# Kernel optimization log

Measured on AMD Instinct MI355X. Metric: run time of the kernel, lower is better.

The kernel has to match this reference:

```python
import jax, jax.numpy as jnp
import numpy as np

B, C, D, H = 16, 64, 512, 8
SEQ_LEN, LABEL_LEN, PRED_LEN = 1024, 512, 512
DEC_LEN = LABEL_LEN + PRED_LEN
DFF, KSIZE, FACTOR = 2048, 25, 3
E_LAYERS, D_LAYERS = 2, 1


def _pos_emb(L, d):
    pos = np.arange(L, dtype=np.float32)[:, None]
    div = np.exp(np.arange(0, d, 2, dtype=np.float32) * (-np.log(10000.0) / d))
    pe = np.zeros((L, d), np.float32)
    pe[:, 0::2] = np.sin(pos * div)
    pe[:, 1::2] = np.cos(pos * div)
    return jnp.asarray(pe)


def moving_mean(x, k=KSIZE):
    # AvgPool1d(k, stride=1) with replicate padding of (k-1)//2 at both ends
    pad = (k - 1) // 2
    xp = jnp.concatenate([jnp.repeat(x[:, :1], pad, 1), x, jnp.repeat(x[:, -1:], pad, 1)], axis=1)
    cs = jnp.cumsum(xp, axis=1)
    cs = jnp.concatenate([jnp.zeros_like(cs[:, :1]), cs], axis=1)
    return (cs[:, k:] - cs[:, :-k]) / k


def series_decomp(x):
    mm = moving_mean(x)
    return x - mm, mm


def circ_conv3(x, W):
    # Conv1d kernel=3, circular padding=1, no bias. x [B,L,Cin], W [3,Cin,Cout]
    L = x.shape[1]
    xp = jnp.concatenate([x[:, -1:], x, x[:, :1]], axis=1)
    return sum(jnp.einsum('blc,cd->bld', xp[:, k:k + L], W[k]) for k in range(3))


def my_layernorm(x, g, b):
    # LayerNorm then subtract per-sample mean over the time axis (special seasonal layernorm)
    mu = x.mean(-1, keepdims=True)
    var = x.var(-1, keepdims=True)
    xh = (x - mu) / jnp.sqrt(var + 1e-5) * g + b
    return xh - xh.mean(axis=1, keepdims=True)


def autocorrelation(q, k, v):
    # q,k,v: [B,L,H,E]. FFT cross-correlation, top-k lag selection, time-delay aggregation.
    L = q.shape[1]
    qf = jnp.fft.rfft(q.transpose(0, 2, 3, 1), axis=-1)
    kf = jnp.fft.rfft(k.transpose(0, 2, 3, 1), axis=-1)
    corr = jnp.fft.irfft(qf * jnp.conj(kf), n=L, axis=-1)  # [B,H,E,L]
    top_k = int(FACTOR * np.log(L))
    w, delay = jax.lax.top_k(corr.mean(axis=(1, 2)), top_k)  # [B,K]
    tc = jax.nn.softmax(w, axis=-1)
    vp = v.transpose(0, 2, 3, 1)  # [B,H,E,L]
    base = jnp.arange(L)
    agg = jnp.zeros_like(vp)
    for i in range(top_k):  # small fixed K (= int(factor*log L) = 20)
        idx = (base[None, :] + delay[:, i:i + 1]) % L  # circular shift == gather on doubled values
        pattern = jnp.take_along_axis(vp, idx[:, None, None, :], axis=-1)
        agg = agg + pattern * tc[:, i][:, None, None, None]
    return agg.transpose(0, 3, 1, 2)  # [B,L,H,E]


def ac_layer(q_in, kv_in, Wq, bq, Wk, bk, Wv, bv, Wo, bo):
    Bb, L, _ = q_in.shape
    S = kv_in.shape[1]
    E = D // H
    q = (q_in @ Wq + bq).reshape(Bb, L, H, E)
    k = (kv_in @ Wk + bk).reshape(Bb, S, H, E)
    v = (kv_in @ Wv + bv).reshape(Bb, S, H, E)
    out = autocorrelation(q, k, v)  # L == S by construction here
    return out.reshape(Bb, L, D) @ Wo + bo


def _forward(x_enc, x_dec, enc_emb_w, dec_emb_w, enc_Wq, enc_bq, enc_Wk, enc_bk, enc_Wv, enc_bv, enc_Wo, enc_bo, enc_ff1, enc_ff2, enc_ng, enc_nb, dsa_Wq, dsa_bq, dsa_Wk, dsa_bk, dsa_Wv, dsa_bv, dsa_Wo, dsa_bo, dca_Wq, dca_bq, dca_Wk, dca_bk, dca_Wv, dca_bv, dca_Wo, dca_bo, dec_ff1, dec_ff2, dec_trend_w, proj_w, proj_b):
    mean = jnp.repeat(x_enc.mean(axis=1, keepdims=True), PRED_LEN, axis=1)
    zeros = jnp.zeros((x_dec.shape[0], PRED_LEN, x_dec.shape[2]), x_enc.dtype)
    seasonal_init, trend_init = series_decomp(x_enc)
    trend = jnp.concatenate([trend_init[:, -LABEL_LEN:], mean], axis=1)
    seasonal_init = jnp.concatenate([seasonal_init[:, -LABEL_LEN:], zeros], axis=1)
    # encoder (DataEmbedding_wo_temp = token circular conv + sinusoidal pos, dropout=0)
    x = circ_conv3(x_enc, enc_emb_w) + _pos_emb(SEQ_LEN, D)[None]
    for l in range(E_LAYERS):
        x = x + ac_layer(x, x, enc_Wq[l], enc_bq[l], enc_Wk[l], enc_bk[l], enc_Wv[l], enc_bv[l], enc_Wo[l], enc_bo[l])
        x, _ = series_decomp(x)
        y = jax.nn.gelu(x @ enc_ff1[l], approximate=False) @ enc_ff2[l]
        x, _ = series_decomp(x + y)
    enc_out = my_layernorm(x, enc_ng, enc_nb)
    # decoder
    xd = circ_conv3(seasonal_init, dec_emb_w) + _pos_emb(DEC_LEN, D)[None]
    for l in range(D_LAYERS):
        xd = xd + ac_layer(xd, xd, dsa_Wq[l], dsa_bq[l], dsa_Wk[l], dsa_bk[l], dsa_Wv[l], dsa_bv[l], dsa_Wo[l], dsa_bo[l])
        xd, t1 = series_decomp(xd)
        xd = xd + ac_layer(xd, enc_out, dca_Wq[l], dca_bq[l], dca_Wk[l], dca_bk[l], dca_Wv[l], dca_bv[l], dca_Wo[l], dca_bo[l])
        xd, t2 = series_decomp(xd)
        y = jax.nn.gelu(xd @ dec_ff1[l], approximate=False) @ dec_ff2[l]
        xd, t3 = series_decomp(xd + y)
        trend = trend + circ_conv3(t1 + t2 + t3, dec_trend_w[l])  # trend projection conv
    seasonal = xd @ proj_w + proj_b
    out = trend + seasonal
    return out[:, -PRED_LEN:]


def setup_inputs():
    key = jax.random.key(0)
    ks = iter(jax.random.split(key, 64))
    def n(shape, s=0.02):
        return jax.random.normal(next(ks), shape, jnp.float32) * s
    inp = {}
    inp['x_enc'] = jax.random.normal(next(ks), (B, SEQ_LEN, C), jnp.float32)
    inp['x_dec'] = jax.random.normal(next(ks), (B, DEC_LEN, C), jnp.float32)
    inp['enc_emb_w'] = n((3, C, D))
    inp['dec_emb_w'] = n((3, C, D))
    for p in ['Wq', 'Wk', 'Wv', 'Wo']:
        bp = p.replace('W', 'b')
        inp['enc_' + p] = n((E_LAYERS, D, D)); inp['enc_' + bp] = jnp.zeros((E_LAYERS, D))
        inp['dsa_' + p] = n((D_LAYERS, D, D)); inp['dsa_' + bp] = jnp.zeros((D_LAYERS, D))
        inp['dca_' + p] = n((D_LAYERS, D, D)); inp['dca_' + bp] = jnp.zeros((D_LAYERS, D))
    inp['enc_ff1'] = n((E_LAYERS, D, DFF)); inp['enc_ff2'] = n((E_LAYERS, DFF, D))
    inp['enc_ng'] = jnp.ones((D,), jnp.float32); inp['enc_nb'] = jnp.zeros((D,), jnp.float32)
    inp['dec_ff1'] = n((D_LAYERS, D, DFF)); inp['dec_ff2'] = n((D_LAYERS, DFF, D))
    inp['dec_trend_w'] = n((D_LAYERS, 3, D, C))
    inp['proj_w'] = n((D, C)); inp['proj_b'] = jnp.zeros((C,), jnp.float32)
    return inp


def reference(x_enc, x_dec, enc_emb_w, dec_emb_w, enc_Wq, enc_bq, enc_Wk, enc_bk, enc_Wv, enc_bv, enc_Wo, enc_bo, enc_ff1, enc_ff2, enc_ng, enc_nb, dsa_Wq, dsa_bq, dsa_Wk, dsa_bk, dsa_Wv, dsa_bv, dsa_Wo, dsa_bo, dca_Wq, dca_bq, dca_Wk, dca_bk, dca_Wv, dca_bv, dca_Wo, dca_bo, dec_ff1, dec_ff2, dec_trend_w, proj_w, proj_b):
    return _forward(x_enc, x_dec, enc_emb_w, dec_emb_w, enc_Wq, enc_bq, enc_Wk, enc_bk, enc_Wv, enc_bv, enc_Wo, enc_bo, enc_ff1, enc_ff2, enc_ng, enc_nb, dsa_Wq, dsa_bq, dsa_Wk, dsa_bk, dsa_Wv, dsa_bv, dsa_Wo, dsa_bo, dca_Wq, dca_bq, dca_Wk, dca_bk, dca_Wv, dca_bv, dca_Wo, dca_bo, dec_ff1, dec_ff2, dec_trend_w, proj_w, proj_b)
```

## Files before the change

### kernel.cpp

```cpp
#include <hip/hip_runtime.h>
#include <math.h>

#define B_   16
#define L_   1024
#define C_   64
#define D_   512
#define DFF_ 2048
#define TOPK_ 20

typedef float f4 __attribute__((ext_vector_type(4)));
typedef float f32x4 __attribute__((ext_vector_type(4)));
typedef short bf16x8 __attribute__((ext_vector_type(8)));
typedef unsigned short u16x8 __attribute__((ext_vector_type(8)));

__device__ __forceinline__ unsigned short f2bf(float f) {
    union { float f; unsigned u; } a; a.f = f;
    unsigned r = a.u + 0x7fff + ((a.u >> 16) & 1);
    return (unsigned short)(r >> 16);
}
__device__ __forceinline__ float bf2f(unsigned short h) {
    union { unsigned u; float f; } a; a.u = ((unsigned)h) << 16;
    return a.f;
}

__device__ __forceinline__ float gelu_fast(float c) {
    float z  = c * 0.70710678118654752f;
    float az = fabsf(z);
    float t  = __builtin_amdgcn_rcpf(fmaf(0.3275911f, az, 1.0f));
    float p  = fmaf(fmaf(fmaf(fmaf(1.061405429f, t, -1.453152027f), t,
                              1.421413741f), t, -0.284496736f), t, 0.254829592f) * t;
    float e  = __expf(-z * z);
    float ea = fmaf(-p, e, 1.0f);
    float er = copysignf(ea, z);
    return 0.5f * c * (1.0f + er);
}

__device__ __forceinline__ void gld16(const void* g, void* l) {
    __builtin_amdgcn_global_load_lds(
        (const __attribute__((address_space(1))) unsigned int*)g,
        (__attribute__((address_space(3))) unsigned int*)l, 16, 0, 0);
}


__global__ __launch_bounds__(256)
void gemm_bf16(const unsigned short* __restrict__ A, const unsigned short* __restrict__ Bt,
               float* __restrict__ Cf, unsigned short* __restrict__ Cb,
               unsigned short* __restrict__ Cl,
               const float* __restrict__ bias, int M, int N, int K, int flags, int nx)
{
    __shared__ unsigned short As0[128 * 32], As1[128 * 32];
    __shared__ unsigned short Bs0[128 * 32], Bs1[128 * 32];
    const int tid = threadIdx.x;
    const int wave = tid >> 6, lane = tid & 63;

    int total = gridDim.x;
    int h = blockIdx.x;
    int lidx = h;
    if ((total & 7) == 0) {
        int q = total >> 3;
        lidx = (h & 7) * q + (h >> 3);
    }
    const int bm = (lidx / nx) * 128, bn = (lidx % nx) * 128;
    const int wm = (wave >> 1) << 6, wn = (wave & 1) << 6;

    const int r0 = (wave << 5) + (lane >> 2);
    const int kq = (((lane & 3) ^ ((lane >> 3) & 3)) << 3);
    const unsigned short* Ap0 = A + (size_t)(bm + r0) * K + kq;
    const unsigned short* Ap1 = Ap0 + (size_t)16 * K;
    const unsigned short* Bp0 = Bt + (size_t)(bn + r0) * K + kq;
    const unsigned short* Bp1 = Bp0 + (size_t)16 * K;
    const int wo0 = (wave << 5) * 32, wo1 = ((wave << 5) + 16) * 32;

    const int la = lane & 15, h4 = lane >> 4;
    const int sw = (la >> 1) & 3;
    f32x4 acc[4][4] = {};

    for (int k0 = 0; k0 < K; k0 += 64) {
        gld16(Ap0 + k0, &As0[wo0]);      gld16(Ap1 + k0, &As0[wo1]);
        gld16(Bp0 + k0, &Bs0[wo0]);      gld16(Bp1 + k0, &Bs0[wo1]);
        gld16(Ap0 + k0 + 32, &As1[wo0]); gld16(Ap1 + k0 + 32, &As1[wo1]);
        gld16(Bp0 + k0 + 32, &Bs1[wo0]); gld16(Bp1 + k0 + 32, &Bs1[wo1]);
        __syncthreads();
        bf16x8 a[4], b[4];
#pragma unroll
        for (int i = 0; i < 4; ++i) {
            a[i] = *(const bf16x8*)&As0[(wm + i * 16 + la) * 32 + ((h4 ^ sw) << 3)];
            b[i] = *(const bf16x8*)&Bs0[(wn + i * 16 + la) * 32 + ((h4 ^ sw) << 3)];
        }
#pragma unroll
        for (int mi = 0; mi < 4; ++mi)
#pragma unroll
            for (int ni = 0; ni < 4; ++ni)
                acc[mi][ni] = __builtin_amdgcn_mfma_f32_16x16x32_bf16(a[mi], b[ni], acc[mi][ni], 0, 0, 0);
#pragma unroll
        for (int i = 0; i < 4; ++i) {
            a[i] = *(const bf16x8*)&As1[(wm + i * 16 + la) * 32 + ((h4 ^ sw) << 3)];
            b[i] = *(const bf16x8*)&Bs1[(wn + i * 16 + la) * 32 + ((h4 ^ sw) << 3)];
        }
#pragma unroll
        for (int mi = 0; mi < 4; ++mi)
#pragma unroll
            for (int ni = 0; ni < 4; ++ni)
                acc[mi][ni] = __builtin_amdgcn_mfma_f32_16x16x32_bf16(a[mi], b[ni], acc[mi][ni], 0, 0, 0);
        __syncthreads();
    }

#pragma unroll
    for (int mi = 0; mi < 4; ++mi) {
#pragma unroll
        for (int r = 0; r < 4; ++r) {
            int m = bm + wm + mi * 16 + h4 * 4 + r;
#pragma unroll
            for (int ni = 0; ni < 4; ++ni) {
                int n = bn + wn + ni * 16 + la;
                float c = acc[mi][ni][r];
                if (bias) c += bias[n];
                if (flags & 2) c = gelu_fast(c);
                size_t o = (size_t)m * N + n;
                if (Cf) { if (flags & 1) Cf[o] += c; else Cf[o] = c; }
                if (Cb) {
                    unsigned short hb = f2bf(c);
                    Cb[o] = hb;
                    if (Cl) Cl[o] = f2bf(c - bf2f(hb));
                }
            }
        }
    }
}

__global__ __launch_bounds__(512)
void gemm256_gelu(const unsigned short* __restrict__ A, const unsigned short* __restrict__ Bt,
                  unsigned short* __restrict__ Cb, int M, int N, int K, int nx)
{
    __shared__ unsigned short As[2][16384];
    __shared__ unsigned short Bs[2][16384];
    const int tid = threadIdx.x;
    const int wave = tid >> 6, lane = tid & 63;

    int total = gridDim.x;
    int h = blockIdx.x;
    int lidx = h;
    if ((total & 7) == 0) {
        int q = total >> 3;
        lidx = (h & 7) * q + (h >> 3);
    }
    const int bm = (lidx / nx) * 256, bn = (lidx % nx) * 256;
    const int wm = (wave >> 2) << 7, wn = (wave & 3) << 6;

    const int r0 = (wave << 5) + (lane >> 2);
    const int kq = (((lane & 3) ^ ((lane >> 3) & 3)) << 3);
    const unsigned short* Ap0 = A + (size_t)(bm + r0) * K + kq;
    const unsigned short* Ap1 = Ap0 + (size_t)16 * K;
    const unsigned short* Bp0 = Bt + (size_t)(bn + r0) * K + kq;
    const unsigned short* Bp1 = Bp0 + (size_t)16 * K;
    const int wo0 = (wave << 5) * 32, wo1 = ((wave << 5) + 16) * 32;

    const int la = lane & 15, h4 = lane >> 4;
    const int sw = (la >> 1) & 3;
    f32x4 acc[8][4] = {};

    gld16(Ap0, &As[0][wo0]);             gld16(Ap1, &As[0][wo1]);
    gld16(Bp0, &Bs[0][wo0]);             gld16(Bp1, &Bs[0][wo1]);
    gld16(Ap0 + 32, &As[0][8192 + wo0]); gld16(Ap1 + 32, &As[0][8192 + wo1]);
    gld16(Bp0 + 32, &Bs[0][8192 + wo0]); gld16(Bp1 + 32, &Bs[0][8192 + wo1]);
    __syncthreads();

    const int nt = K >> 6;
    for (int t = 0; t < nt; ++t) {
        if (t + 1 < nt) {
            const int k0 = (t + 1) << 6;
            const int nb2 = (t + 1) & 1;
            gld16(Ap0 + k0, &As[nb2][wo0]);             gld16(Ap1 + k0, &As[nb2][wo1]);
            gld16(Bp0 + k0, &Bs[nb2][wo0]);             gld16(Bp1 + k0, &Bs[nb2][wo1]);
            gld16(Ap0 + k0 + 32, &As[nb2][8192 + wo0]); gld16(Ap1 + k0 + 32, &As[nb2][8192 + wo1]);
            gld16(Bp0 + k0 + 32, &Bs[nb2][8192 + wo0]); gld16(Bp1 + k0 + 32, &Bs[nb2][8192 + wo1]);
        }
        const int cb = t & 1;
#pragma unroll
        for (int hh = 0; hh < 2; ++hh) {
            const int hb = hh << 13;
            bf16x8 a[8], b[4];
#pragma unroll
            for (int i = 0; i < 8; ++i)
                a[i] = *(const bf16x8*)&As[cb][hb + (wm + i * 16 + la) * 32 + ((h4 ^ sw) << 3)];
#pragma unroll
            for (int i = 0; i < 4; ++i)
                b[i] = *(const bf16x8*)&Bs[cb][hb + (wn + i * 16 + la) * 32 + ((h4 ^ sw) << 3)];
#pragma unroll
            for (int mi = 0; mi < 8; ++mi)
#pragma unroll
                for (int ni = 0; ni < 4; ++ni)
                    acc[mi][ni] = __builtin_amdgcn_mfma_f32_16x16x32_bf16(a[mi], b[ni], acc[mi][ni], 0, 0, 0);
        }
        __syncthreads();
    }

#pragma unroll
    for (int mi = 0; mi < 8; ++mi)
#pragma unroll
        for (int r = 0; r < 4; ++r) {
            int m = bm + wm + mi * 16 + h4 * 4 + r;
#pragma unroll
            for (int ni = 0; ni < 4; ++ni) {
                int n = bn + wn + ni * 16 + la;
                Cb[(size_t)m * N + n] = f2bf(gelu_fast(acc[mi][ni][r]));
            }
        }
}

__global__ __launch_bounds__(256)
void gemm_split(const unsigned short* __restrict__ A, const unsigned short* __restrict__ Bt,
                unsigned short* __restrict__ o0h, unsigned short* __restrict__ o0l, const float* __restrict__ b0,
                unsigned short* __restrict__ o1h, unsigned short* __restrict__ o1l, const float* __restrict__ b1,
                unsigned short* __restrict__ o2h, unsigned short* __restrict__ o2l, const float* __restrict__ b2,
                float* __restrict__ Gz, int M, int N, int K, int nx)
{
    __shared__ unsigned short As0[128 * 32], As1[128 * 32];
    __shared__ unsigned short Bs0[128 * 32], Bs1[128 * 32];
    const int tid = threadIdx.x;
    const int wave = tid >> 6, lane = tid & 63;

    int total = gridDim.x;
    int h = blockIdx.x;
    if (Gz && h < 64) Gz[h * 256 + tid] = 0.f;
    int lidx = h;
    if ((total & 7) == 0) {
        int q = total >> 3;
        lidx = (h & 7) * q + (h >> 3);
    }
    const int bm = (lidx / nx) * 128, bn = (lidx % nx) * 128;
    const int wm = (wave >> 1) << 6, wn = (wave & 1) << 6;

    const int sel = bn >> 9;
    unsigned short* oh = sel == 0 ? o0h : (sel == 1 ? o1h : o2h);
    unsigned short* ol = sel == 0 ? o0l : (sel == 1 ? o1l : o2l);
    const float* bias  = sel == 0 ? b0  : (sel == 1 ? b1  : b2);
    const int nb = bn & 511;

    const int r0 = (wave << 5) + (lane >> 2);
    const int kq = (((lane & 3) ^ ((lane >> 3) & 3)) << 3);
    const unsigned short* Ap0 = A + (size_t)(bm + r0) * K + kq;
    const unsigned short* Ap1 = Ap0 + (size_t)16 * K;
    const unsigned short* Bp0 = Bt + (size_t)(bn + r0) * K + kq;
    const unsigned short* Bp1 = Bp0 + (size_t)16 * K;
    const int wo0 = (wave << 5) * 32, wo1 = ((wave << 5) + 16) * 32;

    const int la = lane & 15, h4 = lane >> 4;
    const int sw = (la >> 1) & 3;
    f32x4 acc[4][4] = {};

    for (int k0 = 0; k0 < K; k0 += 64) {
        gld16(Ap0 + k0, &As0[wo0]);      gld16(Ap1 + k0, &As0[wo1]);
        gld16(Bp0 + k0, &Bs0[wo0]);      gld16(Bp1 + k0, &Bs0[wo1]);
        gld16(Ap0 + k0 + 32, &As1[wo0]); gld16(Ap1 + k0 + 32, &As1[wo1]);
        gld16(Bp0 + k0 + 32, &Bs1[wo0]); gld16(Bp1 + k0 + 32, &Bs1[wo1]);
        __syncthreads();
        bf16x8 a[4], b[4];
#pragma unroll
        for (int i = 0; i < 4; ++i) {
            a[i] = *(const bf16x8*)&As0[(wm + i * 16 + la) * 32 + ((h4 ^ sw) << 3)];
            b[i] = *(const bf16x8*)&Bs0[(wn + i * 16 + la) * 32 + ((h4 ^ sw) << 3)];
        }
#pragma unroll
        for (int mi = 0; mi < 4; ++mi)
#pragma unroll
            for (int ni = 0; ni < 4; ++ni)
                acc[mi][ni] = __builtin_amdgcn_mfma_f32_16x16x32_bf16(a[mi], b[ni], acc[mi][ni], 0, 0, 0);
#pragma unroll
        for (int i = 0; i < 4; ++i) {
            a[i] = *(const bf16x8*)&As1[(wm + i * 16 + la) * 32 + ((h4 ^ sw) << 3)];
            b[i] = *(const bf16x8*)&Bs1[(wn + i * 16 + la) * 32 + ((h4 ^ sw) << 3)];
        }
#pragma unroll
        for (int mi = 0; mi < 4; ++mi)
#pragma unroll
            for (int ni = 0; ni < 4; ++ni)
                acc[mi][ni] = __builtin_amdgcn_mfma_f32_16x16x32_bf16(a[mi], b[ni], acc[mi][ni], 0, 0, 0);
        __syncthreads();
    }

#pragma unroll
    for (int mi = 0; mi < 4; ++mi) {
#pragma unroll
        for (int r = 0; r < 4; ++r) {
            int m = bm + wm + mi * 16 + h4 * 4 + r;
#pragma unroll
            for (int ni = 0; ni < 4; ++ni) {
                int n2 = nb + wn + ni * 16 + la;
                float c = acc[mi][ni][r] + bias[n2];
                size_t o = (size_t)m * 512 + n2;
                unsigned short hb = f2bf(c);
                oh[o] = hb;
                if (ol) ol[o] = f2bf(c - bf2f(hb));
            }
        }
    }
}

__global__ __launch_bounds__(256)
void tcast_kernel(const float* __restrict__ W, unsigned short* __restrict__ Wt, int R, int Cc)
{
    __shared__ float t[32][33];
    int bx = blockIdx.x * 32, by = blockIdx.y * 32;
    int tx = threadIdx.x & 31, ty = threadIdx.x >> 5;
#pragma unroll
    for (int i = 0; i < 32; i += 8)
        t[ty + i][tx] = W[(size_t)(by + ty + i) * Cc + bx + tx];
    __syncthreads();
#pragma unroll
    for (int i = 0; i < 32; i += 8)
        Wt[(size_t)(bx + ty + i) * R + by + tx] = f2bf(t[tx][ty + i]);
}

struct P16 { const float* p[16]; };
__global__ __launch_bounds__(256)
void tcast_all(P16 srcs, unsigned short* __restrict__ dst)
{
    __shared__ float t[32][33];
    const float* W = srcs.p[blockIdx.z];
    unsigned short* Wt = dst + (size_t)blockIdx.z * 262144;
    int bx = blockIdx.x * 32, by = blockIdx.y * 32;
    int tx = threadIdx.x & 31, ty = threadIdx.x >> 5;
#pragma unroll
    for (int i = 0; i < 32; i += 8)
        t[ty + i][tx] = W[(size_t)(by + ty + i) * 512 + bx + tx];
    __syncthreads();
#pragma unroll
    for (int i = 0; i < 32; i += 8)
        Wt[(size_t)(bx + ty + i) * 512 + by + tx] = f2bf(t[tx][ty + i]);
}

__global__ __launch_bounds__(256)
void pegen_kernel(float* __restrict__ PE)
{
    int idx = blockIdx.x * blockDim.x + threadIdx.x;
    int n = idx & 511, l = idx >> 9;
    int i2 = n & ~1;
    float div = expf(-(float)i2 * 0.017988946039015984f);
    float ang = (float)l * div;
    PE[idx] = (n & 1) ? cosf(ang) : sinf(ang);
}

__global__ __launch_bounds__(256)
void emb_kernel(const float* __restrict__ A, const float* __restrict__ W,
                const float* __restrict__ PEt,
                float* __restrict__ Xo, unsigned short* __restrict__ Xb)
{
    __shared__ float As[66][68];
    __shared__ float Ws[3][64][64];
    const int tid = threadIdx.x;
    const int bn = blockIdx.x * 64, bm = blockIdx.y * 64;
    const int base = bm & ~1023;
    for (int i = tid; i < 66 * 64; i += 256) {
        int r = i >> 6, c = i & 63;
        int l = (bm - base) + r - 1;
        if (l < 0) l += 1024; else if (l >= 1024) l -= 1024;
        As[r][c] = A[(size_t)(base + l) * 64 + c];
    }
    for (int i = tid; i < 3 * 64 * 64; i += 256) {
        int tap = i >> 12, rem = i & 4095, k = rem >> 6, c = rem & 63;
        Ws[tap][k][c] = W[((size_t)tap * 64 + k) * 512 + bn + c];
    }
    __syncthreads();
    const int tx = tid & 15, ty = tid >> 4;
    float acc[4][4] = {};
    for (int tap = 0; tap < 3; ++tap)
        for (int k = 0; k < 64; ++k) {
            f4 bv = *(const f4*)&Ws[tap][k][tx * 4];
#pragma unroll
            for (int i = 0; i < 4; ++i) {
                float a = As[ty * 4 + i + tap][k];
#pragma unroll
                for (int j = 0; j < 4; ++j)
                    acc[i][j] = fmaf(a, bv[j], acc[i][j]);
            }
        }
#pragma unroll
    for (int i = 0; i < 4; ++i) {
        int m = bm + ty * 4 + i;
        int l = m & 1023;
#pragma unroll
        for (int j = 0; j < 4; ++j) {
            int n = bn + tx * 4 + j;
            float c = acc[i][j] + PEt[((size_t)l << 9) + n];
            size_t o = (size_t)m * 512 + n;
            Xo[o] = c;
            Xb[o] = f2bf(c);
        }
    }
}

__global__ __launch_bounds__(256)
void tail_kernel(const float* __restrict__ TSUM, const float* __restrict__ T1,
                 const float* __restrict__ Wt, const float* __restrict__ pw,
                 float* __restrict__ PC, float* __restrict__ PP)
{
    __shared__ float Ts[18][17];
    __shared__ float T1s[16][17];
    __shared__ float Ws[3][16][64];
    __shared__ float Ps[16][64];
    const int tid = threadIdx.x;
    const int bo = blockIdx.x * 16;
    const int kc = blockIdx.y;
    const int b = bo >> 9;
    const int lbase = (bo & 511) + 512;
    const size_t rowbase = (size_t)b << 10;
    const int tc4 = (tid & 15) * 4;
    const int tr = tid >> 4;
    const int kbeg = kc * 64, kend = kbeg + 64;
    float cacc[4] = {}, pacc[4] = {};

    for (int k0 = kbeg; k0 < kend; k0 += 16) {
        for (int i = tid; i < 18 * 16; i += 256) {
            int r = i >> 4, c = i & 15;
            int l = lbase + r - 1; if (l >= 1024) l -= 1024;
            Ts[r][c] = TSUM[(rowbase + l) * 512 + k0 + c];
        }
        {
            int r = tid >> 4, c = tid & 15;
            T1s[r][c] = T1[(rowbase + lbase + r) * 512 + k0 + c];
        }
        for (int i = tid; i < 3 * 16 * 16; i += 256) {
            int tap = i / 256, rem = i & 255, k = rem >> 4, c4 = (rem & 15) * 4;
            *(f4*)&Ws[tap][k][c4] = *(const f4*)&Wt[((size_t)tap * 512 + k0 + k) * 64 + c4];
        }
        if (tid < 256) {
            int k = tid >> 4, c4 = (tid & 15) * 4;
            *(f4*)&Ps[k][c4] = *(const f4*)&pw[(size_t)(k0 + k) * 64 + c4];
        }
        __syncthreads();
        for (int tap = 0; tap < 3; ++tap)
#pragma unroll
            for (int k = 0; k < 16; ++k) {
                f4 bv = *(const f4*)&Ws[tap][k][tc4];
                float a = Ts[tr + tap][k];
#pragma unroll
                for (int j = 0; j < 4; ++j)
                    cacc[j] = fmaf(a, bv[j], cacc[j]);
            }
#pragma unroll
        for (int k = 0; k < 16; ++k) {
            f4 bv = *(const f4*)&Ps[k][tc4];
            float a = T1s[tr][k];
#pragma unroll
            for (int j = 0; j < 4; ++j)
                pacc[j] = fmaf(a, bv[j], pacc[j]);
        }
        __syncthreads();
    }
    size_t o = ((size_t)kc * 8192 + (bo + tr)) * 64 + tc4;
    *(f4*)&PC[o] = *(f4*)cacc;
    *(f4*)&PP[o] = *(f4*)pacc;
}

__global__ __launch_bounds__(256)
void tailred_kernel(const float* __restrict__ PC, const float* __restrict__ PP,
                    const float* __restrict__ MEANC, const float* __restrict__ pb,
                    float* __restrict__ OUT)
{
    int idx = blockIdx.x * blockDim.x + threadIdx.x;
    int n = idx & 63;
    int b = idx >> 15;
    const size_t S = (size_t)8192 * 64;
    float cs = PC[idx];
    float ps = PP[idx];
#pragma unroll
    for (int s = 1; s < 8; ++s) {
        cs += PC[s * S + idx];
        ps += PP[s * S + idx];
    }
    OUT[idx] = (MEANC[(b << 6) + n] + cs) + (ps + pb[n]);
}

__global__ __launch_bounds__(256)
void corr_mfma(const unsigned short* __restrict__ Qh, const unsigned short* __restrict__ Ql,
               const unsigned short* __restrict__ Kh, const unsigned short* __restrict__ Kl,
               float* __restrict__ G)
{
    __shared__ unsigned short Qhs[128 * 32], Qls[128 * 32], Khs[128 * 32], Kls[128 * 32];
    __shared__ float diagw[4][256];
    const int tid = threadIdx.x;
    const int wave = tid >> 6, lane = tid & 63;

    const int i_ = blockIdx.x;
    const int x_ = i_ & 7, j_ = i_ >> 3;
    const int b = x_ + ((j_ >> 6) << 3);
    const int tile = j_ & 63;
    const int bt = (tile >> 3) * 128, bs = (tile & 7) * 128;

    const int wm = (wave >> 1) << 6, wn = (wave & 1) << 6;
    const size_t boff = (size_t)b << 19;

    const int r0 = (wave << 5) + (lane >> 2);
    const int kq = (((lane & 3) ^ ((lane >> 3) & 3)) << 3);
    const size_t g0 = boff + (size_t)(bt + r0) * 512 + kq;
    const size_t g1 = g0 + (size_t)16 * 512;
    const size_t p0 = boff + (size_t)(bs + r0) * 512 + kq;
    const size_t p1 = p0 + (size_t)16 * 512;
    unsigned short* qh0 = &Qhs[(wave << 5) * 32]; unsigned short* qh1 = &Qhs[((wave << 5) + 16) * 32];
    unsigned short* ql0 = &Qls[(wave << 5) * 32]; unsigned short* ql1 = &Qls[((wave << 5) + 16) * 32];
    unsigned short* kh0 = &Khs[(wave << 5) * 32]; unsigned short* kh1 = &Khs[((wave << 5) + 16) * 32];
    unsigned short* kl0 = &Kls[(wave << 5) * 32]; unsigned short* kl1 = &Kls[((wave << 5) + 16) * 32];

    float* dz = &diagw[0][0];
    dz[tid] = 0.f; dz[tid + 256] = 0.f; dz[tid + 512] = 0.f; dz[tid + 768] = 0.f;

    const int la = lane & 15, h4 = lane >> 4;
    const int sw = (la >> 1) & 3;
    f32x4 acc[4][4] = {};

    for (int k0 = 0; k0 < 512; k0 += 32) {
        gld16(Qh + g0 + k0, qh0); gld16(Qh + g1 + k0, qh1);
        gld16(Ql + g0 + k0, ql0); gld16(Ql + g1 + k0, ql1);
        gld16(Kh + p0 + k0, kh0); gld16(Kh + p1 + k0, kh1);
        gld16(Kl + p0 + k0, kl0); gld16(Kl + p1 + k0, kl1);
        __syncthreads();
        bf16x8 ah[4], al[4], bh[4], bl[4];
#pragma unroll
        for (int i = 0; i < 4; ++i) {
            int ro = (wm + i * 16 + la) * 32 + ((h4 ^ sw) << 3);
            int co = (wn + i * 16 + la) * 32 + ((h4 ^ sw) << 3);
            ah[i] = *(const bf16x8*)&Qhs[ro];
            al[i] = *(const bf16x8*)&Qls[ro];
            bh[i] = *(const bf16x8*)&Khs[co];
            bl[i] = *(const bf16x8*)&Kls[co];
        }
#pragma unroll
        for (int mi = 0; mi < 4; ++mi)
#pragma unroll
            for (int ni = 0; ni < 4; ++ni) {
                acc[mi][ni] = __builtin_amdgcn_mfma_f32_16x16x32_bf16(ah[mi], bh[ni], acc[mi][ni], 0, 0, 0);
                acc[mi][ni] = __builtin_amdgcn_mfma_f32_16x16x32_bf16(ah[mi], bl[ni], acc[mi][ni], 0, 0, 0);
                acc[mi][ni] = __builtin_amdgcn_mfma_f32_16x16x32_bf16(al[mi], bh[ni], acc[mi][ni], 0, 0, 0);
            }
        __syncthreads();
    }

    float rbin[7][4] = {};
#pragma unroll
    for (int mi = 0; mi < 4; ++mi)
#pragma unroll
        for (int ni = 0; ni < 4; ++ni)
#pragma unroll
            for (int r = 0; r < 4; ++r)
                rbin[mi - ni + 3][r] += acc[mi][ni][r];

    const int base = (wm - wn) + 4 * h4 - la + 127;
#pragma unroll
    for (int d = 0; d < 7; ++d)
#pragma unroll
        for (int r = 0; r < 4; ++r)
            atomicAdd(&diagw[wave][base + 16 * (d - 3) + r], rbin[d][r]);
    __syncthreads();
    if (tid < 255) {
        float s = diagw[0][tid] + diagw[1][tid] + diagw[2][tid] + diagw[3][tid];
        int n = (bt - bs + tid - 127) & 1023;
        atomicAdd(&G[(b << 10) + n], s);
    }
}

__global__ __launch_bounds__(256)
void topk_kernel(const float* __restrict__ G, int* __restrict__ delay,
                 float* __restrict__ tc)
{
    __shared__ float vals[1024];
    __shared__ float pw[4];
    __shared__ int   pwi[4];
    __shared__ float wsel[TOPK_];
    __shared__ int   isel[TOPK_];
    const int b = blockIdx.x, tid = threadIdx.x;
    const int lane = tid & 63, wid = tid >> 6;
    for (int i = tid; i < 1024; i += 256) vals[i] = G[(b << 10) + i] * (1.0f / 512.0f);
    __syncthreads();
    for (int it = 0; it < TOPK_; ++it) {
        float bv = -INFINITY; int bi = 0;
#pragma unroll
        for (int u = 0; u < 4; ++u) {
            int i = tid * 4 + u;
            float v = vals[i];
            if (v > bv) { bv = v; bi = i; }
        }
#pragma unroll
        for (int o = 32; o > 0; o >>= 1) {
            float ov = __shfl_xor(bv, o, 64);
            int   oi = __shfl_xor(bi, o, 64);
            if (ov > bv || (ov == bv && oi < bi)) { bv = ov; bi = oi; }
        }
        if (lane == 0) { pw[wid] = bv; pwi[wid] = bi; }
        __syncthreads();
        if (tid == 0) {
            float m = pw[0]; int mi = pwi[0];
#pragma unroll
            for (int t = 1; t < 4; ++t)
                if (pw[t] > m || (pw[t] == m && pwi[t] < mi)) { m = pw[t]; mi = pwi[t]; }
            wsel[it] = m; isel[it] = mi;
            vals[mi] = -INFINITY;
        }
        __syncthreads();
    }
    if (tid == 0) {
        float m = wsel[0];
#pragma unroll
        for (int i = 1; i < TOPK_; ++i) m = fmaxf(m, wsel[i]);
        float e[TOPK_], s = 0.f;
#pragma unroll
        for (int i = 0; i < TOPK_; ++i) { e[i] = expf(wsel[i] - m); s += e[i]; }
        float inv = 1.0f / s;
#pragma unroll
        for (int i = 0; i < TOPK_; ++i) {
            tc[b * TOPK_ + i] = e[i] * inv;
            delay[b * TOPK_ + i] = isel[i];
        }
    }
}

__global__ __launch_bounds__(256)
void agg_kernel(const unsigned short* __restrict__ V, const int* __restrict__ delay,
                const float* __restrict__ tc, unsigned short* __restrict__ out)
{
    __shared__ int   dls[TOPK_];
    __shared__ float tcs[TOPK_];
    int h = blockIdx.x, g = gridDim.x, lh = h;
    if ((g & 7) == 0) {
        int q = g >> 3;
        lh = (h & 7) * q + (h >> 3);
    }
    int idx = (lh * blockDim.x + threadIdx.x) * 8;
    int d = idx & 511;
    int l = (idx >> 9) & 1023;
    int b = idx >> 19;
    if (threadIdx.x < TOPK_) {
        dls[threadIdx.x] = delay[b * TOPK_ + threadIdx.x];
        tcs[threadIdx.x] = tc[b * TOPK_ + threadIdx.x];
    }
    __syncthreads();
    const unsigned short* Vb = V + ((size_t)b << 19);
    float s[8] = {};
#pragma unroll
    for (int i = 0; i < TOPK_; ++i) {
        int row = (l + dls[i]) & 1023;
        float w = tcs[i];
        u16x8 v = *(const u16x8*)&Vb[((size_t)row << 9) + d];
#pragma unroll
        for (int j = 0; j < 8; ++j)
            s[j] = fmaf(w, bf2f(v[j]), s[j]);
    }
    u16x8 o;
#pragma unroll
    for (int j = 0; j < 8; ++j) o[j] = f2bf(s[j]);
    *(u16x8*)&out[idx] = o;
}

__global__ void decomp_kernel(const float* __restrict__ x, float* __restrict__ seas,
                              unsigned short* __restrict__ seasb,
                              float* __restrict__ trend, int Bn, int Ln, int Ch,
                              int nseg, int tmode)
{
    int h = blockIdx.x, g = gridDim.x, lh = h;
    if ((g & 7) == 0) {
        int q = g >> 3;
        lh = (h & 7) * q + (h >> 3);
    }
    int idx = lh * blockDim.x + threadIdx.x;
    int total = Bn * Ch * nseg;
    if (idx >= total) return;
    int ch = idx % Ch;
    int rest = idx / Ch;
    int seg = rest % nseg;
    int b = rest / nseg;
    int segL = Ln / nseg;
    int l0 = seg * segL;
    const float* xp = x + (size_t)b * Ln * Ch + ch;
    float* sp = seas + (size_t)b * Ln * Ch + ch;
    unsigned short* bp = seasb ? seasb + (size_t)b * Ln * Ch + ch : nullptr;
    float* tp = trend ? trend + (size_t)b * Ln * Ch + ch : nullptr;
    float s = 0.f;
    for (int j = -12; j <= 12; ++j) {
        int t = l0 + j;
        t = t < 0 ? 0 : (t > Ln - 1 ? Ln - 1 : t);
        s += xp[(size_t)t * Ch];
    }
    for (int l = l0; l < l0 + segL; ++l) {
        float mm = s * (1.0f / 25.0f);
        float v = xp[(size_t)l * Ch] - mm;
        sp[(size_t)l * Ch] = v;
        if (bp) bp[(size_t)l * Ch] = f2bf(v);
        if (tmode == 1) tp[(size_t)l * Ch] = mm;
        else if (tmode == 2) tp[(size_t)l * Ch] += mm;
        int ta = l + 13; if (ta > Ln - 1) ta = Ln - 1;
        int ts = l - 12; if (ts < 0) ts = 0;
        s += xp[(size_t)ta * Ch] - xp[(size_t)ts * Ch];
    }
}

__global__ __launch_bounds__(256)
void lnrow_kernel(const float* __restrict__ x, const float* __restrict__ g,
                  const float* __restrict__ bv, float* __restrict__ out)
{
    __shared__ float sh1[4], sh2[4];
    int row = blockIdx.x, tid = threadIdx.x;
    const float* xr = x + ((size_t)row << 9);
    float v0 = xr[tid], v1 = xr[tid + 256];
    float s = v0 + v1, q = v0 * v0 + v1 * v1;
#pragma unroll
    for (int o = 32; o > 0; o >>= 1) {
        s += __shfl_down(s, o, 64);
        q += __shfl_down(q, o, 64);
    }
    int wid = tid >> 6;
    if ((tid & 63) == 0) { sh1[wid] = s; sh2[wid] = q; }
    __syncthreads();
    if (tid == 0) {
        sh1[0] = sh1[0] + sh1[1] + sh1[2] + sh1[3];
        sh2[0] = sh2[0] + sh2[1] + sh2[2] + sh2[3];
    }
    __syncthreads();
    float mu = sh1[0] * (1.0f / 512.0f);
    float var = sh2[0] * (1.0f / 512.0f) - mu * mu;
    float inv = rsqrtf(var + 1e-5f);
    out[((size_t)row << 9) + tid] = (v0 - mu) * inv * g[tid] + bv[tid];
    out[((size_t)row << 9) + tid + 256] = (v1 - mu) * inv * g[tid + 256] + bv[tid + 256];
}

__global__ void colmean_kernel(const float* __restrict__ x, float* __restrict__ m)
{
    int idx = blockIdx.x * blockDim.x + threadIdx.x;
    if (idx >= B_ * D_) return;
    int b = idx >> 9, d = idx & 511;
    const float* xp = x + ((size_t)b << 19) + d;
    float s = 0.f;
    for (int l = 0; l < L_; ++l) s += xp[(size_t)l << 9];
    m[idx] = s * (1.0f / 1024.0f);
}

__global__ void colsub_kernel(const float* __restrict__ x, const float* __restrict__ m,
                              unsigned short* __restrict__ out)
{
    int idx = blockIdx.x * blockDim.x + threadIdx.x;
    int d = idx & 511;
    int b = idx >> 19;
    out[idx] = f2bf(x[idx] - m[(b << 9) + d]);
}

__global__ void meanx_kernel(const float* __restrict__ x, float* __restrict__ m)
{
    int idx = blockIdx.x * blockDim.x + threadIdx.x;
    if (idx >= B_ * C_) return;
    int b = idx >> 6, c = idx & 63;
    const float* xp = x + (size_t)b * L_ * C_ + c;
    float s = 0.f;
    for (int l = 0; l < L_; ++l) s += xp[(size_t)l << 6];
    m[idx] = s * (1.0f / 1024.0f);
}

__global__ void builddec_kernel(const float* __restrict__ seenc, float* __restrict__ seasin)
{
    int idx = blockIdx.x * blockDim.x + threadIdx.x;
    int c = idx & 63;
    int l = (idx >> 6) & 1023;
    int b = idx >> 16;
    if (l < 512) {
        int src = (b << 16) + ((512 + l) << 6) + c;
        seasin[idx] = seenc[src];
    } else {
        seasin[idx] = 0.f;
    }
}

extern "C" void kernel_launch(void* const* d_in, const int* in_sizes, int n_in,
                              void* d_out, int out_size, void* d_ws, size_t ws_size,
                              hipStream_t stream)
{
    auto F = [&](int i) { return (const float*)d_in[i]; };
    const float* x_enc     = F(0);
    const float* enc_emb_w = F(2);
    const float* dec_emb_w = F(3);
    const float* enc_Wq = F(4);  const float* enc_bq = F(5);
    const float* dsa_Wq = F(6);  const float* dsa_bq = F(7);
    const float* dca_Wq = F(8);  const float* dca_bq = F(9);
    const float* enc_Wk = F(10); const float* enc_bk = F(11);
    const float* dsa_Wk = F(12); const float* dsa_bk = F(13);
    const float* dca_Wk = F(14); const float* dca_bk = F(15);
    const float* enc_Wv = F(16); const float* enc_bv = F(17);
    const float* dsa_Wv = F(18); const float* dsa_bv = F(19);
    const float* dca_Wv = F(20); const float* dca_bv = F(21);
    const float* enc_Wo = F(22); const float* enc_bo = F(23);
    const float* dsa_Wo = F(24); const float* dsa_bo = F(25);
    const float* dca_Wo = F(26); const float* dca_bo = F(27);
    const float* enc_ff1 = F(28); const float* enc_ff2 = F(29);
    const float* enc_ng = F(30);  const float* enc_nb = F(31);
    const float* dec_ff1 = F(32); const float* dec_ff2 = F(33);
    const float* dec_trend_w = F(34);
    const float* proj_w = F(35);  const float* proj_b = F(36);

    constexpr size_t F512 = (size_t)B_ * L_ * D_;
    constexpr size_t F64  = (size_t)B_ * L_ * C_;
    constexpr size_t SMALL = 1024 + 16384 + 320 + 320 + 8192;
    constexpr size_t WTSA_N = 16 * 262144;
    constexpr size_t WTSF_N = 2 * 1024 * 1024;
    size_t need = (3 * F512 + 2 * F64 + SMALL) * 4 + (8 * F512 + WTSA_N + WTSF_N) * 2;
    if (ws_size < need) return;

    float* X      = (float*)d_ws;
    float* T1     = X + F512;
    float* TSUM   = T1 + F512;
    float* SEASIN = TSUM + F512;
    float* PET    = SEASIN + F64;
    float* MEANC  = PET + F64;
    float* G      = MEANC + 1024;
    float* TCW    = G + 16384;
    int*   DEL    = (int*)(TCW + 320);
    float* LNMEAN = (float*)(DEL + 320);
    unsigned short* AB   = (unsigned short*)(LNMEAN + 8192);
    unsigned short* EB   = AB + F512;
    unsigned short* VB   = EB + F512;
    unsigned short* HB   = VB + F512;
    unsigned short* QHI  = HB + F512;
    unsigned short* QLO  = QHI + F512;
    unsigned short* KHI  = QLO + F512;
    unsigned short* KLO  = KHI + F512;
    unsigned short* WTSA = KLO + F512;
    unsigned short* WTSF = WTSA + WTSA_N;
    float* OUT = (float*)d_out;

    const int M = B_ * L_;

    auto mgemm = [&](const unsigned short* A, const unsigned short* Bt, float* Cf,
                     unsigned short* Cb, unsigned short* Cl, const float* bias,
                     int Mm, int Nn, int Kk, int flags) {
        int nx = Nn / 128;
        int total = nx * (Mm / 128);
        gemm_bf16<<<total, 256, 0, stream>>>(A, Bt, Cf, Cb, Cl, bias, Mm, Nn, Kk, flags, nx);
    };
    auto tcast = [&](const float* W, unsigned short* Wt, int R, int Cc) {
        tcast_kernel<<<dim3(Cc / 32, R / 32), 256, 0, stream>>>(W, Wt, R, Cc);
    };
    auto corr_topk_agg = [&]() {
        corr_mfma<<<1024, 256, 0, stream>>>(QHI, QLO, KHI, KLO, G);
        topk_kernel<<<16, 256, 0, stream>>>(G, DEL, TCW);
        agg_kernel<<<(int)(F512 / 8 / 256), 256, 0, stream>>>(VB, DEL, TCW, HB);
    };
    auto attn_self = [&](const unsigned short* xin, int slotbase,
                         const float* bq, const float* bk, const float* bvp, const float* bo,
                         float* resid) {
        gemm_split<<<12 * 128, 256, 0, stream>>>(xin, WTSA + (size_t)slotbase * 262144,
            QHI, QLO, bq, KHI, KLO, bk, VB, nullptr, bvp, G, M, 1536, 512, 12);
        corr_topk_agg();
        mgemm(HB, WTSA + (size_t)(slotbase + 3) * 262144, resid, nullptr, nullptr, bo, M, 512, 512, 1);
    };
    auto attn_cross = [&](const unsigned short* qin, const unsigned short* kvin, int slotbase,
                          const float* bq, const float* bk, const float* bvp, const float* bo,
                          float* resid) {
        mgemm(qin, WTSA + (size_t)slotbase * 262144, nullptr, QHI, QLO, bq, M, 512, 512, 0);
        gemm_split<<<8 * 128, 256, 0, stream>>>(kvin, WTSA + (size_t)(slotbase + 1) * 262144,
            KHI, KLO, bk, VB, nullptr, bvp, nullptr, nullptr, nullptr, G, M, 1024, 512, 8);
        corr_topk_agg();
        mgemm(HB, WTSA + (size_t)(slotbase + 3) * 262144, resid, nullptr, nullptr, bo, M, 512, 512, 1);
    };
    auto ffblock = [&](const unsigned short* xin, const float* W1, const float* W2, float* resid) {
        unsigned short* Wf1 = WTSF;
        unsigned short* Wf2 = WTSF + 1048576;
        unsigned short* HFULL = QHI;
        tcast(W1, Wf1, 512, 2048);
        tcast(W2, Wf2, 2048, 512);
        gemm256_gelu<<<512, 512, 0, stream>>>(xin, Wf1, HFULL, M, 2048, 512, 8);
        mgemm(HFULL, Wf2, resid, nullptr, nullptr, nullptr, M, 512, 2048, 1);
    };

    {
        P16 srcs;
        for (int l = 0; l < 2; ++l) {
            srcs.p[l * 4 + 0] = enc_Wq + (size_t)l * 262144;
            srcs.p[l * 4 + 1] = enc_Wk + (size_t)l * 262144;
            srcs.p[l * 4 + 2] = enc_Wv + (size_t)l * 262144;
            srcs.p[l * 4 + 3] = enc_Wo + (size_t)l * 262144;
        }
        srcs.p[8]  = dsa_Wq; srcs.p[9]  = dsa_Wk; srcs.p[10] = dsa_Wv; srcs.p[11] = dsa_Wo;
        srcs.p[12] = dca_Wq; srcs.p[13] = dca_Wk; srcs.p[14] = dca_Wv; srcs.p[15] = dca_Wo;
        tcast_all<<<dim3(16, 16, 16), 256, 0, stream>>>(srcs, WTSA);
    }
    pegen_kernel<<<2048, 256, 0, stream>>>(PET);

    float* SEENC = (float*)QHI;
    decomp_kernel<<<(B_ * C_ * 64 + 255) / 256, 256, 0, stream>>>(x_enc, SEENC, nullptr, nullptr, B_, L_, C_, 64, 0);
    meanx_kernel<<<(B_ * C_ + 255) / 256, 256, 0, stream>>>(x_enc, MEANC);
    builddec_kernel<<<(int)(F64 / 256), 256, 0, stream>>>(SEENC, SEASIN);

    emb_kernel<<<dim3(8, 256), 256, 0, stream>>>(x_enc, enc_emb_w, PET, X, AB);

    for (int l = 0; l < 2; ++l) {
        attn_self(AB, l * 4,
                  enc_bq + l * D_, enc_bk + l * D_, enc_bv + l * D_, enc_bo + l * D_, X);
        decomp_kernel<<<(B_ * D_ * 64 + 255) / 256, 256, 0, stream>>>(X, T1, AB, nullptr, B_, L_, D_, 64, 0);
        ffblock(AB, enc_ff1 + (size_t)l * D_ * DFF_, enc_ff2 + (size_t)l * DFF_ * D_, T1);
        decomp_kernel<<<(B_ * D_ * 64 + 255) / 256, 256, 0, stream>>>(T1, X, AB, nullptr, B_, L_, D_, 64, 0);
    }
    lnrow_kernel<<<M, 256, 0, stream>>>(X, enc_ng, enc_nb, T1);
    colmean_kernel<<<(B_ * D_ + 255) / 256, 256, 0, stream>>>(T1, LNMEAN);
    colsub_kernel<<<(int)(F512 / 256), 256, 0, stream>>>(T1, LNMEAN, EB);

    float* XD = X;
    emb_kernel<<<dim3(8, 256), 256, 0, stream>>>(SEASIN, dec_emb_w, PET, XD, AB);

    attn_self(AB, 8, dsa_bq, dsa_bk, dsa_bv, dsa_bo, XD);
    decomp_kernel<<<(B_ * D_ * 64 + 255) / 256, 256, 0, stream>>>(XD, T1, AB, TSUM, B_, L_, D_, 64, 1);

    attn_cross(AB, EB, 12, dca_bq, dca_bk, dca_bv, dca_bo, T1);
    decomp_kernel<<<(B_ * D_ * 64 + 255) / 256, 256, 0, stream>>>(T1, XD, AB, TSUM, B_, L_, D_, 64, 2);

    ffblock(AB, dec_ff1, dec_ff2, XD);
    decomp_kernel<<<(B_ * D_ * 64 + 255) / 256, 256, 0, stream>>>(XD, T1, nullptr, TSUM, B_, L_, D_, 64, 2);

    float* PART_C = (float*)QHI;
    float* PART_P = PART_C + (size_t)8 * 8192 * 64;
    tail_kernel<<<dim3(512, 8), 256, 0, stream>>>(TSUM, T1, dec_trend_w, proj_w, PART_C, PART_P);
    tailred_kernel<<<2048, 256, 0, stream>>>(PART_C, PART_P, MEANC, proj_b, OUT);
}
```

Baseline: 1.727 ms.

## Enlarge corr_mfma tile to 256x256 with double-buffered LDS prefetch

The correlation MFMA kernel now uses 512-thread blocks computing 256x256 tiles, with eight waves each owning 128x64, instead of 128x128 tiles. Each block fetches the next K slice into a second LDS buffer while computing on the current one, so only one barrier per iteration remains. The aim is to raise data reuse per global load, hide load latency, and reduce diagonal atomic traffic to G. In exchange, per-thread accumulator registers double and LDS use rises, while only 256 blocks are launched, which may lower occupancy and how many CUs are kept busy.

```diff
diff --git a/kernel.cpp b/kernel.cpp
--- a/kernel.cpp
+++ b/kernel.cpp
@@ -472,23 +472,23 @@
     OUT[idx] = (MEANC[(b << 6) + n] + cs) + (ps + pb[n]);
 }
 
-__global__ __launch_bounds__(256)
+__global__ __launch_bounds__(512)
 void corr_mfma(const unsigned short* __restrict__ Qh, const unsigned short* __restrict__ Ql,
                const unsigned short* __restrict__ Kh, const unsigned short* __restrict__ Kl,
                float* __restrict__ G)
 {
-    __shared__ unsigned short Qhs[128 * 32], Qls[128 * 32], Khs[128 * 32], Kls[128 * 32];
-    __shared__ float diagw[4][256];
+    __shared__ unsigned short Qhs[2][8192], Qls[2][8192], Khs[2][8192], Kls[2][8192];
+    __shared__ float diagw[8][512];
     const int tid = threadIdx.x;
     const int wave = tid >> 6, lane = tid & 63;
 
     const int i_ = blockIdx.x;
     const int x_ = i_ & 7, j_ = i_ >> 3;
-    const int b = x_ + ((j_ >> 6) << 3);
-    const int tile = j_ & 63;
-    const int bt = (tile >> 3) * 128, bs = (tile & 7) * 128;
-
-    const int wm = (wave >> 1) << 6, wn = (wave & 1) << 6;
+    const int b = x_ + ((j_ >> 4) << 3);
+    const int tile = j_ & 15;
+    const int bt = (tile >> 2) * 256, bs = (tile & 3) * 256;
+
+    const int wm = (wave >> 2) << 7, wn = (wave & 3) << 6;
     const size_t boff = (size_t)b << 19;
 
     const int r0 = (wave << 5) + (lane >> 2);
@@ -497,64 +497,92 @@
     const size_t g1 = g0 + (size_t)16 * 512;
     const size_t p0 = boff + (size_t)(bs + r0) * 512 + kq;
     const size_t p1 = p0 + (size_t)16 * 512;
-    unsigned short* qh0 = &Qhs[(wave << 5) * 32]; unsigned short* qh1 = &Qhs[((wave << 5) + 16) * 32];
-    unsigned short* ql0 = &Qls[(wave << 5) * 32]; unsigned short* ql1 = &Qls[((wave << 5) + 16) * 32];
-    unsigned short* kh0 = &Khs[(wave << 5) * 32]; unsigned short* kh1 = &Khs[((wave << 5) + 16) * 32];
-    unsigned short* kl0 = &Kls[(wave << 5) * 32]; unsigned short* kl1 = &Kls[((wave << 5) + 16) * 32];
-
-    float* dz = &diagw[0][0];
-    dz[tid] = 0.f; dz[tid + 256] = 0.f; dz[tid + 512] = 0.f; dz[tid + 768] = 0.f;
+    const int wo0 = (wave << 5) * 32, wo1 = ((wave << 5) + 16) * 32;
+
+    {
+        float* dz = &diagw[0][0];
+#pragma unroll
+        for (int i = 0; i < 8; ++i) dz[tid + i * 512] = 0.f;
+    }
 
     const int la = lane & 15, h4 = lane >> 4;
     const int sw = (la >> 1) & 3;
-    f32x4 acc[4][4] = {};
-
-    for (int k0 = 0; k0 < 512; k0 += 32) {
-        gld16(Qh + g0 + k0, qh0); gld16(Qh + g1 + k0, qh1);
-        gld16(Ql + g0 + k0, ql0); gld16(Ql + g1 + k0, ql1);
-        gld16(Kh + p0 + k0, kh0); gld16(Kh + p1 + k0, kh1);
-        gld16(Kl + p0 + k0, kl0); gld16(Kl + p1 + k0, kl1);
+    f32x4 acc[8][4] = {};
+
+    gld16(Qh + g0, &Qhs[0][wo0]); gld16(Qh + g1, &Qhs[0][wo1]);
+    gld16(Ql + g0, &Qls[0][wo0]); gld16(Ql + g1, &Qls[0][wo1]);
+    gld16(Kh + p0, &Khs[0][wo0]); gld16(Kh + p1, &Khs[0][wo1]);
+    gld16(Kl + p0, &Kls[0][wo0]); gld16(Kl + p1, &Kls[0][wo1]);
+    __syncthreads();
+
+    for (int t = 0; t < 16; ++t) {
+        if (t + 1 < 16) {
+            const int k0 = (t + 1) << 5;
+            const int nb2 = (t + 1) & 1;
+            gld16(Qh + g0 + k0, &Qhs[nb2][wo0]); gld16(Qh + g1 + k0, &Qhs[nb2][wo1]);
+            gld16(Ql + g0 + k0, &Qls[nb2][wo0]); gld16(Ql + g1 + k0, &Qls[nb2][wo1]);
+            gld16(Kh + p0 + k0, &Khs[nb2][wo0]); gld16(Kh + p1 + k0, &Khs[nb2][wo1]);
+            gld16(Kl + p0 + k0, &Kls[nb2][wo0]); gld16(Kl + p1 + k0, &Kls[nb2][wo1]);
+        }
+        const int cb = t & 1;
+        bf16x8 ah[8], bh[4];
+#pragma unroll
+        for (int i = 0; i < 8; ++i)
+            ah[i] = *(const bf16x8*)&Qhs[cb][(wm + i * 16 + la) * 32 + ((h4 ^ sw) << 3)];
+#pragma unroll
+        for (int i = 0; i < 4; ++i)
+            bh[i] = *(const bf16x8*)&Khs[cb][(wn + i * 16 + la) * 32 + ((h4 ^ sw) << 3)];
+#pragma unroll
+        for (int mi = 0; mi < 8; ++mi)
+#pragma unroll
+            for (int ni = 0; ni < 4; ++ni)
+                acc[mi][ni] = __builtin_amdgcn_mfma_f32_16x16x32_bf16(ah[mi], bh[ni], acc[mi][ni], 0, 0, 0);
+        {
+            bf16x8 bl[4];
+#pragma unroll
+            for (int i = 0; i < 4; ++i)
+                bl[i] = *(const bf16x8*)&Kls[cb][(wn + i * 16 + la) * 32 + ((h4 ^ sw) << 3)];
+#pragma unroll
+            for (int mi = 0; mi < 8; ++mi)
+#pragma unroll
+                for (int ni = 0; ni < 4; ++ni)
+                    acc[mi][ni] = __builtin_amdgcn_mfma_f32_16x16x32_bf16(ah[mi], bl[ni], acc[mi][ni], 0, 0, 0);
+        }
+        {
+            bf16x8 al[8];
+#pragma unroll
+            for (int i = 0; i < 8; ++i)
+                al[i] = *(const bf16x8*)&Qls[cb][(wm + i * 16 + la) * 32 + ((h4 ^ sw) << 3)];
+#pragma unroll
+            for (int mi = 0; mi < 8; ++mi)
+#pragma unroll
+                for (int ni = 0; ni < 4; ++ni)
+                    acc[mi][ni] = __builtin_amdgcn_mfma_f32_16x16x32_bf16(al[mi], bh[ni], acc[mi][ni], 0, 0, 0);
+        }
         __syncthreads();
-        bf16x8 ah[4], al[4], bh[4], bl[4];
-#pragma unroll
-        for (int i = 0; i < 4; ++i) {
-            int ro = (wm + i * 16 + la) * 32 + ((h4 ^ sw) << 3);
-            int co = (wn + i * 16 + la) * 32 + ((h4 ^ sw) << 3);
-            ah[i] = *(const bf16x8*)&Qhs[ro];
-            al[i] = *(const bf16x8*)&Qls[ro];
-            bh[i] = *(const bf16x8*)&Khs[co];
-            bl[i] = *(const bf16x8*)&Kls[co];
-        }
-#pragma unroll
-        for (int mi = 0; mi < 4; ++mi)
-#pragma unroll
-            for (int ni = 0; ni < 4; ++ni) {
-                acc[mi][ni] = __builtin_amdgcn_mfma_f32_16x16x32_bf16(ah[mi], bh[ni], acc[mi][ni], 0, 0, 0);
-                acc[mi][ni] = __builtin_amdgcn_mfma_f32_16x16x32_bf16(ah[mi], bl[ni], acc[mi][ni], 0, 0, 0);
-                acc[mi][ni] = __builtin_amdgcn_mfma_f32_16x16x32_bf16(al[mi], bh[ni], acc[mi][ni], 0, 0, 0);
-            }
-        __syncthreads();
-    }
-
-    float rbin[7][4] = {};
-#pragma unroll
-    for (int mi = 0; mi < 4; ++mi)
+    }
+
+    float rbin[11][4] = {};
+#pragma unroll
+    for (int mi = 0; mi < 8; ++mi)
 #pragma unroll
         for (int ni = 0; ni < 4; ++ni)
 #pragma unroll
             for (int r = 0; r < 4; ++r)
                 rbin[mi - ni + 3][r] += acc[mi][ni][r];
 
-    const int base = (wm - wn) + 4 * h4 - la + 127;
-#pragma unroll
-    for (int d = 0; d < 7; ++d)
+    const int base = (wm - wn) + 4 * h4 - la + 255;
+#pragma unroll
+    for (int d = 0; d < 11; ++d)
 #pragma unroll
         for (int r = 0; r < 4; ++r)
             atomicAdd(&diagw[wave][base + 16 * (d - 3) + r], rbin[d][r]);
     __syncthreads();
-    if (tid < 255) {
-        float s = diagw[0][tid] + diagw[1][tid] + diagw[2][tid] + diagw[3][tid];
-        int n = (bt - bs + tid - 127) & 1023;
+    if (tid < 511) {
+        float s = 0.f;
+#pragma unroll
+        for (int w = 0; w < 8; ++w) s += diagw[w][tid];
+        int n = (bt - bs + tid - 255) & 1023;
         atomicAdd(&G[(b << 10) + n], s);
     }
 }
@@ -836,7 +864,7 @@
         tcast_kernel<<<dim3(Cc / 32, R / 32), 256, 0, stream>>>(W, Wt, R, Cc);
     };
     auto corr_topk_agg = [&]() {
-        corr_mfma<<<1024, 256, 0, stream>>>(QHI, QLO, KHI, KLO, G);
+        corr_mfma<<<256, 512, 0, stream>>>(QHI, QLO, KHI, KLO, G);
         topk_kernel<<<16, 256, 0, stream>>>(G, DEL, TCW);
         agg_kernel<<<(int)(F512 / 8 / 256), 256, 0, stream>>>(VB, DEL, TCW, HB);
     };
```

After: 1.676 ms (median of 2 runs). 3.0% less time.
